# Kernel tuning notes

Measured on AMD Instinct MI355X. Metric: run time of the kernel, lower is better.

The kernel has to match this reference:

```python
import jax, jax.numpy as jnp
import numpy as np
from jax import lax

L = 2048        # leaves per tree
VOCAB = 50000
IN_DIM = 300
MEM = 150
HID = 50
NCLS = 5


def _balanced_tree(n_leaf):
    # children-before-parent topological order; node ids: [0, n_leaf) leaves,
    # [n_leaf, 2*n_leaf-1) internal, last id is the root's single child (ROOT is passthrough).
    level = list(range(n_leaf)); nid = n_leaf; lefts = []; rights = []
    while len(level) > 1:
        nxt = []
        for j in range(0, len(level) - 1, 2):
            lefts.append(level[j]); rights.append(level[j + 1]); nxt.append(nid); nid += 1
        if len(level) % 2:
            nxt.append(level[-1])
        level = nxt
    return np.asarray(lefts, np.int32), np.asarray(rights, np.int32)


def setup_inputs() -> dict:
    key = jax.random.key(0)
    ks = jax.random.split(key, 12)
    left, right = _balanced_tree(L)
    s = 0.05
    return {
        "l_tokens": jax.random.randint(ks[0], (L,), 0, VOCAB, dtype=jnp.int32),
        "r_tokens": jax.random.randint(ks[1], (L,), 0, VOCAB, dtype=jnp.int32),
        "left_idx": jnp.asarray(left),
        "right_idx": jnp.asarray(right),
        "emb": jax.random.normal(ks[2], (VOCAB, IN_DIM), jnp.float32) * s,
        "W_ioux": jax.random.normal(ks[3], (IN_DIM, 3 * MEM), jnp.float32) * s,
        "b_ioux": jnp.zeros((3 * MEM,), jnp.float32),
        "W_iouh": jax.random.normal(ks[4], (MEM, 3 * MEM), jnp.float32) * s,
        "b_iouh": jnp.zeros((3 * MEM,), jnp.float32),
        "W_fx": jax.random.normal(ks[5], (IN_DIM, MEM), jnp.float32) * s,
        "b_fx": jnp.zeros((MEM,), jnp.float32),
        "W_fh": jax.random.normal(ks[6], (MEM, MEM), jnp.float32) * s,
        "b_fh": jnp.zeros((MEM,), jnp.float32),
        "W_attn": jax.random.normal(ks[7], (2 * MEM, MEM), jnp.float32) * s,
        "b_attn": jnp.zeros((MEM,), jnp.float32),
        "W_wh": jax.random.normal(ks[8], (2 * MEM, HID), jnp.float32) * s,
        "b_wh": jnp.zeros((HID,), jnp.float32),
        "W_wp": jax.random.normal(ks[9], (HID, NCLS), jnp.float32) * s,
        "b_wp": jnp.zeros((NCLS,), jnp.float32),
    }


def _gates(iou):
    i, o, u = jnp.split(iou, 3, axis=-1)
    return jax.nn.sigmoid(i), jax.nn.sigmoid(o), jnp.tanh(u)


def _tree_lstm(tokens, left, right, emb, W_ioux, b_ioux, W_iouh, b_iouh, W_fh, b_fh):
    # Leaves (child_c = child_h = 0): iou = ioux(x) + iouh(0); fc term vanishes.
    x = emb[tokens]                                   # [L, in_dim]
    i, o, u = _gates(x @ W_ioux + b_ioux + b_iouh)
    c_leaf = i * u
    h_leaf = o * jnp.tanh(c_leaf)
    n_leaf = tokens.shape[0]
    N = 2 * n_leaf - 1
    C = jnp.zeros((N, MEM), x.dtype).at[:n_leaf].set(c_leaf)
    H = jnp.zeros((N, MEM), x.dtype).at[:n_leaf].set(h_leaf)

    # Internal nodes (inputs=None branch): iou = iouh(sum h_child); f_k = sigmoid(fh(h_k)).
    def step(carry, inp):
        C, H = carry
        k, li, ri = inp
        hl, hr = H[li], H[ri]
        i, o, u = _gates((hl + hr) @ W_iouh + b_iouh)
        fl = jax.nn.sigmoid(hl @ W_fh + b_fh)
        fr = jax.nn.sigmoid(hr @ W_fh + b_fh)
        c = i * u + fl * C[li] + fr * C[ri]
        h = o * jnp.tanh(c)
        return (C.at[k].set(c), H.at[k].set(h)), None

    ids = jnp.arange(n_leaf, N, dtype=jnp.int32)
    (C, H), _ = lax.scan(step, (C, H), (ids, left, right))
    return H  # [N, MEM]; H[-1] is the root hidden state (ROOT is passthrough)


def reference(l_tokens, r_tokens, left_idx, right_idx, emb, W_ioux, b_ioux, W_iouh, b_iouh, W_fx, b_fx, W_fh, b_fh, W_attn, b_attn, W_wh, b_wh, W_wp, b_wp):
    Hl = _tree_lstm(l_tokens, left_idx, right_idx, emb, W_ioux, b_ioux, W_iouh, b_iouh, W_fh, b_fh)
    Hr = _tree_lstm(r_tokens, left_idx, right_idx, emb, W_ioux, b_ioux, W_iouh, b_iouh, W_fh, b_fh)
    # Soft cross-attention over all node hidden states (torch code builds [Nr,Nl,m] beta;
    # here expressed as matmuls -- identical math).
    scores = Hl @ Hr.T                               # [Nl, Nr]
    beta_sum = jax.nn.softmax(scores, axis=1) @ Hr    # [Nl, MEM]
    alpha_sum = jax.nn.softmax(scores.T, axis=1) @ Hl  # [Nr, MEM]
    v_l = jnp.concatenate([Hl, beta_sum], axis=1) @ W_attn + b_attn
    v_r = jnp.concatenate([Hr, alpha_sum], axis=1) @ W_attn + b_attn
    lh = v_l[-1:]  # root hidden (root_idx is the root's matched row)
    rh = v_r[-1:]
    feats = jnp.concatenate([lh * rh, jnp.abs(lh - rh)], axis=1)
    hid = jax.nn.sigmoid(feats @ W_wh + b_wh)
    return jax.nn.log_softmax(hid @ W_wp + b_wp, axis=-1)  # [1, NCLS]
```

## Files before the change

kernel.cpp:

```cpp
#include <hip/hip_runtime.h>
#include <math.h>

#define LEAVES 2048
#define NN     4095
#define MEMD   150
#define IOUD   450
#define IND    300
#define STR    152
#define CT     4096


__device__ __forceinline__ float sigf(float x) { return 1.f / (1.f + expf(-x)); }

__global__ __launch_bounds__(256) void k_pack(
    const float* __restrict__ Wh, const float* __restrict__ Wf,
    float4* __restrict__ PWhf)
{
    int i = blockIdx.x * 256 + threadIdx.x;
    if (i < 22500) {
        int k = i / 150, d = i - k * 150;
        float4 v;
        v.x = Wh[k * IOUD + d];
        v.y = Wh[k * IOUD + 150 + d];
        v.z = Wh[k * IOUD + 300 + d];
        v.w = Wf[k * MEMD + d];
        PWhf[i] = v;
    }
}

__global__ __launch_bounds__(320) void k_leaf(
    const int* __restrict__ ltok, const int* __restrict__ rtok,
    const float* __restrict__ emb, const float* __restrict__ Wx,
    const float* __restrict__ bx, const float* __restrict__ bh,
    float* __restrict__ C, float* __restrict__ H)
{
    __shared__ __align__(16) float xs[IND][4];
    __shared__ int tok[4];
    const int tree = blockIdx.y, t = threadIdx.x;
    const int leaf0 = blockIdx.x << 2;
    const int* toks = tree ? rtok : ltok;

    if (t < 4) tok[t] = toks[leaf0 + t];
    __syncthreads();
    if (t < 300) {
        int q = t >> 2, m = t & 3;
        float4 v = *(const float4*)(emb + (size_t)tok[m] * IND + 4 * q);
        xs[4*q+0][m] = v.x; xs[4*q+1][m] = v.y;
        xs[4*q+2][m] = v.z; xs[4*q+3][m] = v.w;
    }
    __syncthreads();

    const int lane = t & 63, w = t >> 6;
    const int kh = lane >> 5;
    const int d  = w * 32 + (lane & 31);
    const bool act = (d < 150);

    float ai[4] = {0.f,0.f,0.f,0.f};
    float ao[4] = {0.f,0.f,0.f,0.f};
    float au[4] = {0.f,0.f,0.f,0.f};

    const float* wp = Wx + (act ? d : 0);
    const int kb = kh * 150;
    #pragma unroll 5
    for (int kk = 0; kk < 150; ++kk) {
        const int k = kb + kk;
        float wi = wp[k * IOUD];
        float wo = wp[k * IOUD + 150];
        float wu = wp[k * IOUD + 300];
        float4 x4 = *(const float4*)(&xs[k][0]);
        float xv[4] = {x4.x, x4.y, x4.z, x4.w};
        #pragma unroll
        for (int m = 0; m < 4; ++m) {
            ai[m] = fmaf(xv[m], wi, ai[m]);
            ao[m] = fmaf(xv[m], wo, ao[m]);
            au[m] = fmaf(xv[m], wu, au[m]);
        }
    }

    #pragma unroll
    for (int m = 0; m < 4; ++m) {
        ai[m] += __shfl_xor(ai[m], 32);
        ao[m] += __shfl_xor(ao[m], 32);
        au[m] += __shfl_xor(au[m], 32);
    }

    if (act && kh == 0) {
        const float bi = bx[d]       + bh[d];
        const float bo = bx[d + 150] + bh[d + 150];
        const float bu = bx[d + 300] + bh[d + 300];
        float* Ct = C + ((size_t)tree * CT + leaf0) * STR;
        float* Ht = H + ((size_t)tree * CT + leaf0) * STR;
        #pragma unroll
        for (int m = 0; m < 4; ++m) {
            float c = sigf(ai[m] + bi) * tanhf(au[m] + bu);
            float h = sigf(ao[m] + bo) * tanhf(c);
            Ct[(size_t)m * STR + d] = c;
            Ht[(size_t)m * STR + d] = h;
        }
    }
}

__global__ __launch_bounds__(640) void k_lvl(
    const float4* __restrict__ PWhf, const float* __restrict__ bh,
    const float* __restrict__ bf,
    float* __restrict__ C, float* __restrict__ H, int PB, int CB)
{
    __shared__ float buf[MEMD][8];
    __shared__ float pb[300][11];
    const int tree = blockIdx.y, t = threadIdx.x;
    const int p0 = blockIdx.x * 4;
    float* Ct = C + (size_t)tree * CT * STR;
    float* Ht = H + (size_t)tree * CT * STR;

    if (t < 600) {
        int m = t / 150, d2 = t - m * 150;
        int cc = CB + 2 * (p0 + m);
        float a = Ht[(size_t)cc * STR + d2];
        float b = Ht[(size_t)(cc + 1) * STR + d2];
        buf[d2][2*m + 0] = a + b;
        buf[d2][2*m + 1] = a;
    }
    __syncthreads();

    const int kh = (t >= 320) ? 1 : 0;
    const int tt = t - 320 * kh;
    const bool act = (tt < 300);
    const int hf = (tt >= 150) ? 1 : 0;
    const int d  = tt - 150 * hf;
    const int m0 = hf * 2;

    float ai[2], ao[2], au[2], afs[2], afl[2], cl[2], cr[2];
    if (act) {
        if (kh == 0) {
            const float bi = bh[d], bo = bh[d + 150], bu = bh[d + 300], bfv = bf[d];
            #pragma unroll
            for (int m = 0; m < 2; ++m) {
                ai[m] = bi; ao[m] = bo; au[m] = bu;
                afs[m] = 2.f * bfv; afl[m] = bfv;
                int cc = CB + 2 * (p0 + m0 + m);
                cl[m] = Ct[(size_t)cc * STR + d];
                cr[m] = Ct[(size_t)(cc + 1) * STR + d];
            }
        } else {
            #pragma unroll
            for (int m = 0; m < 2; ++m) {
                ai[m] = 0.f; ao[m] = 0.f; au[m] = 0.f; afs[m] = 0.f; afl[m] = 0.f;
            }
        }
        const float4* wp = PWhf + d;
        const int kb = kh * 75;
        #pragma unroll 5
        for (int kk = 0; kk < 75; ++kk) {
            const int k = kb + kk;
            float4 w = wp[(size_t)k * 150];
            float4 p4 = *(const float4*)(&buf[k][2 * m0]);
            float hs0 = p4.x, hl0 = p4.y, hs1 = p4.z, hl1 = p4.w;
            ai[0]  = fmaf(hs0, w.x, ai[0]);   ai[1]  = fmaf(hs1, w.x, ai[1]);
            ao[0]  = fmaf(hs0, w.y, ao[0]);   ao[1]  = fmaf(hs1, w.y, ao[1]);
            au[0]  = fmaf(hs0, w.z, au[0]);   au[1]  = fmaf(hs1, w.z, au[1]);
            afs[0] = fmaf(hs0, w.w, afs[0]);  afs[1] = fmaf(hs1, w.w, afs[1]);
            afl[0] = fmaf(hl0, w.w, afl[0]);  afl[1] = fmaf(hl1, w.w, afl[1]);
        }
    }
    if (kh == 1 && act) {
        #pragma unroll
        for (int m = 0; m < 2; ++m) {
            pb[tt][5*m + 0] = ai[m];
            pb[tt][5*m + 1] = ao[m];
            pb[tt][5*m + 2] = au[m];
            pb[tt][5*m + 3] = afs[m];
            pb[tt][5*m + 4] = afl[m];
        }
    }
    __syncthreads();
    if (kh == 0 && act) {
        #pragma unroll
        for (int m = 0; m < 2; ++m) {
            float aiv  = ai[m]  + pb[tt][5*m + 0];
            float aov  = ao[m]  + pb[tt][5*m + 1];
            float auv  = au[m]  + pb[tt][5*m + 2];
            float afsv = afs[m] + pb[tt][5*m + 3];
            float aflv = afl[m] + pb[tt][5*m + 4];
            float frv = afsv - aflv;
            float c = sigf(aiv) * tanhf(auv) + sigf(aflv) * cl[m] + sigf(frv) * cr[m];
            float h = sigf(aov) * tanhf(c);
            size_t rw = (size_t)(PB + p0 + m0 + m) * STR + d;
            Ct[rw] = c;
            Ht[rw] = h;
        }
    }
}

__global__ __launch_bounds__(640) void k_node(
    const float4* __restrict__ PWhf, const float* __restrict__ bh,
    const float* __restrict__ bf,
    float* __restrict__ C, float* __restrict__ H, int PB, int CB)
{
    __shared__ float hsv[MEMD], hlv[MEMD];
    __shared__ float part[4][5][152];
    const int tree = blockIdx.y, node = blockIdx.x, t = threadIdx.x;
    float* Ct = C + (size_t)tree * CT * STR;
    float* Ht = H + (size_t)tree * CT * STR;
    const int c0 = CB + 2 * node;

    if (t < MEMD) {
        float a = Ht[(size_t)c0 * STR + t];
        float b = Ht[(size_t)(c0 + 1) * STR + t];
        hsv[t] = a + b;
        hlv[t] = a;
    }
    __syncthreads();

    const int grp = t / 160, d = t - grp * 160;
    if (d < MEMD) {
        const int k0 = (grp * MEMD) >> 2;
        const int k1 = ((grp + 1) * MEMD) >> 2;
        float ai = 0.f, ao = 0.f, au = 0.f, afs = 0.f, afl = 0.f;
        const float4* wp = PWhf + d;
        #pragma unroll 4
        for (int k = k0; k < k1; ++k) {
            float4 w = wp[(size_t)k * 150];
            float hs = hsv[k], hl = hlv[k];
            ai  = fmaf(hs, w.x, ai);
            ao  = fmaf(hs, w.y, ao);
            au  = fmaf(hs, w.z, au);
            afs = fmaf(hs, w.w, afs);
            afl = fmaf(hl, w.w, afl);
        }
        part[grp][0][d] = ai;  part[grp][1][d] = ao;  part[grp][2][d] = au;
        part[grp][3][d] = afs; part[grp][4][d] = afl;
    }
    __syncthreads();

    if (t < MEMD) {
        const int d2 = t;
        float ai = bh[d2], ao = bh[d2 + 150], au = bh[d2 + 300];
        float bfv = bf[d2];
        float afs = 2.f * bfv, afl = bfv;
        #pragma unroll
        for (int g = 0; g < 4; ++g) {
            ai  += part[g][0][d2]; ao  += part[g][1][d2]; au += part[g][2][d2];
            afs += part[g][3][d2]; afl += part[g][4][d2];
        }
        float cl = Ct[(size_t)c0 * STR + d2];
        float cr = Ct[(size_t)(c0 + 1) * STR + d2];
        float frv = afs - afl;
        float c = sigf(ai) * tanhf(au) + sigf(afl) * cl + sigf(frv) * cr;
        float h = sigf(ao) * tanhf(c);
        size_t rw = (size_t)(PB + node) * STR + d2;
        Ct[rw] = c;
        Ht[rw] = h;
    }
}

__global__ __launch_bounds__(256) void k_attn(
    const float* __restrict__ H, float* __restrict__ cstat, float* __restrict__ part)
{
    __shared__ float lv[MEMD];
    __shared__ float sc[64];
    __shared__ float pv[64];
    const int bid = blockIdx.x, t = threadIdx.x;
    const int side = bid >> 6, chunk = bid & 63;
    const int j0 = chunk << 6;
    const int jn = min(64, NN - j0);
    const float* lastrow = H + ((size_t)side * CT + (NN - 1)) * STR;
    if (t < MEMD) lv[t] = lastrow[t];
    __syncthreads();

    const float* src = H + (size_t)(side ^ 1) * CT * STR + (size_t)j0 * STR;
    const int wave = t >> 6, lane = t & 63;
    for (int r = wave; r < jn; r += 4) {
        const float* row = src + (size_t)r * STR;
        float a = lv[lane] * row[lane] + lv[lane + 64] * row[lane + 64];
        if (lane < 22) a += lv[lane + 128] * row[lane + 128];
        #pragma unroll
        for (int off = 32; off; off >>= 1) a += __shfl_xor(a, off);
        if (lane == 0) sc[r] = a;
    }
    __syncthreads();
    if (wave == 0) {
        float v = (lane < jn) ? sc[lane] : -3.4e38f;
        float m = v;
        #pragma unroll
        for (int off = 32; off; off >>= 1) m = fmaxf(m, __shfl_xor(m, off));
        float e = (lane < jn) ? expf(v - m) : 0.f;
        pv[lane] = e;
        float s = e;
        #pragma unroll
        for (int off = 32; off; off >>= 1) s += __shfl_xor(s, off);
        if (lane == 0) {
            cstat[(side * 64 + chunk) * 2 + 0] = m;
            cstat[(side * 64 + chunk) * 2 + 1] = s;
        }
    }
    __syncthreads();
    if (t < MEMD) {
        float a = 0.f;
        for (int j = 0; j < jn; ++j) a += pv[j] * src[(size_t)j * STR + t];
        part[(size_t)(side * 64 + chunk) * STR + t] = a;
    }
}

__global__ __launch_bounds__(512) void k_final(
    const float* __restrict__ H, const float* __restrict__ cstat,
    const float* __restrict__ part,
    const float* __restrict__ Wattn, const float* __restrict__ battn,
    const float* __restrict__ Wwh, const float* __restrict__ bwh,
    const float* __restrict__ Wwp, const float* __restrict__ bwp,
    float* __restrict__ outp)
{
    __shared__ float scl[2][64];
    __shared__ float gseS[2];
    __shared__ float ba[300], catl[300], catr[300], vl[150], vr[150];
    __shared__ float feats[300], hid[50], logits[5];
    const int t = threadIdx.x, wave = t >> 6, lane = t & 63;

    if (wave < 2) {
        float lm = cstat[(wave * 64 + lane) * 2 + 0];
        float ls = cstat[(wave * 64 + lane) * 2 + 1];
        float m = lm;
        #pragma unroll
        for (int off = 32; off; off >>= 1) m = fmaxf(m, __shfl_xor(m, off));
        float s = expf(lm - m);
        scl[wave][lane] = s;
        float se = ls * s;
        #pragma unroll
        for (int off = 32; off; off >>= 1) se += __shfl_xor(se, off);
        if (lane == 0) gseS[wave] = se;
    }
    __syncthreads();
    if (t < 300) {
        int side = t / MEMD, d = t - side * MEMD;
        float a = 0.f;
        for (int c = 0; c < 64; ++c)
            a += part[(size_t)(side * 64 + c) * STR + d] * scl[side][c];
        ba[t] = a / gseS[side];
    }
    __syncthreads();
    const float* Hl_last = H + (size_t)(0 * CT + NN - 1) * STR;
    const float* Hr_last = H + (size_t)(1 * CT + NN - 1) * STR;
    if (t < MEMD) {
        catl[t] = Hl_last[t]; catl[150 + t] = ba[t];
        catr[t] = Hr_last[t]; catr[150 + t] = ba[150 + t];
    }
    __syncthreads();
    if (t < 300) {
        int d = (t < 150) ? t : t - 150;
        const float* cat = (t < 150) ? catl : catr;
        float a = battn[d];
        for (int k = 0; k < 300; ++k) a = fmaf(cat[k], Wattn[k * 150 + d], a);
        if (t < 150) vl[d] = a; else vr[d] = a;
    }
    __syncthreads();
    if (t < MEMD) {
        feats[t] = vl[t] * vr[t];
        feats[150 + t] = fabsf(vl[t] - vr[t]);
    }
    __syncthreads();
    if (t < 50) {
        float a = bwh[t];
        for (int k = 0; k < 300; ++k) a = fmaf(feats[k], Wwh[k * 50 + t], a);
        hid[t] = sigf(a);
    }
    __syncthreads();
    if (t < 5) {
        float a = bwp[t];
        for (int g = 0; g < 50; ++g) a = fmaf(hid[g], Wwp[g * 5 + t], a);
        logits[t] = a;
    }
    __syncthreads();
    if (t == 0) {
        float m = logits[0];
        for (int c = 1; c < 5; ++c) m = fmaxf(m, logits[c]);
        float s = 0.f;
        for (int c = 0; c < 5; ++c) s += expf(logits[c] - m);
        float lse = m + logf(s);
        for (int c = 0; c < 5; ++c) outp[c] = logits[c] - lse;
    }
}

extern "C" void kernel_launch(void* const* d_in, const int* in_sizes, int n_in,
                              void* d_out, int out_size, void* d_ws, size_t ws_size,
                              hipStream_t stream)
{
    const int*   ltok  = (const int*)d_in[0];
    const int*   rtok  = (const int*)d_in[1];
    const float* emb   = (const float*)d_in[4];
    const float* Wx    = (const float*)d_in[5];
    const float* bx    = (const float*)d_in[6];
    const float* Wh    = (const float*)d_in[7];
    const float* bh    = (const float*)d_in[8];
    const float* Wf    = (const float*)d_in[11];
    const float* bf    = (const float*)d_in[12];
    const float* Wattn = (const float*)d_in[13];
    const float* battn = (const float*)d_in[14];
    const float* Wwh   = (const float*)d_in[15];
    const float* bwh   = (const float*)d_in[16];
    const float* Wwp   = (const float*)d_in[17];
    const float* bwp   = (const float*)d_in[18];
    float* out = (float*)d_out;

    float* ws    = (float*)d_ws;
    float*  C    = ws;
    float*  H    = C + (size_t)2 * CT * STR;
    float*  cs   = H + (size_t)2 * CT * STR;
    float*  part = cs + 256;
    float4* PWhf = (float4*)(part + (size_t)128 * STR);

    k_pack<<<dim3(88), dim3(256), 0, stream>>>(Wh, Wf, PWhf);

    k_leaf<<<dim3(512, 2), dim3(320), 0, stream>>>(ltok, rtok, emb, Wx, bx, bh, C, H);

    k_lvl<<<dim3(256, 2), dim3(640), 0, stream>>>(PWhf, bh, bf, C, H, 2048, 0);
    k_lvl<<<dim3(128, 2), dim3(640), 0, stream>>>(PWhf, bh, bf, C, H, 3072, 2048);
    k_lvl<<<dim3(64,  2), dim3(640), 0, stream>>>(PWhf, bh, bf, C, H, 3584, 3072);

    k_node<<<dim3(128, 2), dim3(640), 0, stream>>>(PWhf, bh, bf, C, H, 3840, 3584);
    k_node<<<dim3(64,  2), dim3(640), 0, stream>>>(PWhf, bh, bf, C, H, 3968, 3840);
    k_node<<<dim3(32,  2), dim3(640), 0, stream>>>(PWhf, bh, bf, C, H, 4032, 3968);
    k_node<<<dim3(16,  2), dim3(640), 0, stream>>>(PWhf, bh, bf, C, H, 4064, 4032);
    k_node<<<dim3(8,   2), dim3(640), 0, stream>>>(PWhf, bh, bf, C, H, 4080, 4064);
    k_node<<<dim3(4,   2), dim3(640), 0, stream>>>(PWhf, bh, bf, C, H, 4088, 4080);
    k_node<<<dim3(2,   2), dim3(640), 0, stream>>>(PWhf, bh, bf, C, H, 4092, 4088);
    k_node<<<dim3(1,   2), dim3(640), 0, stream>>>(PWhf, bh, bf, C, H, 4094, 4092);

    k_attn<<<dim3(128), dim3(256), 0, stream>>>(H, cs, part);
    k_final<<<dim3(1), dim3(512), 0, stream>>>(H, cs, part, Wattn, battn,
                                               Wwh, bwh, Wwp, bwp, out);
}
```

Measured before the change: 155.3 us.

## Compute leaf input projection as bf16 MFMA GEMM with separate activation pass

Replaces the fused fp32 leaf kernel with a pipeline: pack Wx into bf16 MFMA B-fragment layout, gather and convert token embeddings to bf16, run a 16x16x32 bf16 MFMA GEMM into an fp32 IOU buffer, then apply the gate activations in a separate kernel. The aim is to move the 4096x300x450 leaf projection from scalar FMAs onto the matrix cores. In exchange it adds two extra launches and an intermediate IOU round trip through global memory, and lowers input precision to bf16, which may affect accuracy.

```diff
diff --git a/kernel.cpp b/kernel.cpp
--- a/kernel.cpp
+++ b/kernel.cpp
@@ -8,13 +8,25 @@
 #define IND    300
 #define STR    152
 #define CT     4096
-
+#define NT     29
+#define KT     10
+#define IOUSTR 464
 
 __device__ __forceinline__ float sigf(float x) { return 1.f / (1.f + expf(-x)); }
 
-__global__ __launch_bounds__(256) void k_pack(
+__device__ __forceinline__ unsigned short f2bf(float v) {
+    union { float f; unsigned u; } x; x.f = v;
+    unsigned r = x.u + 0x7fffu + ((x.u >> 16) & 1u);
+    return (unsigned short)(r >> 16);
+}
+
+typedef short bf16x8 __attribute__((ext_vector_type(8)));
+typedef float f32x4  __attribute__((ext_vector_type(4)));
+
+__global__ __launch_bounds__(256) void k_pack2(
     const float* __restrict__ Wh, const float* __restrict__ Wf,
-    float4* __restrict__ PWhf)
+    const float* __restrict__ Wx,
+    float4* __restrict__ PWhf, unsigned short* __restrict__ PB)
 {
     int i = blockIdx.x * 256 + threadIdx.x;
     if (i < 22500) {
@@ -25,85 +37,94 @@
         v.z = Wh[k * IOUD + 300 + d];
         v.w = Wf[k * MEMD + d];
         PWhf[i] = v;
-    }
-}
-
-__global__ __launch_bounds__(320) void k_leaf(
+    } else if (i < 22500 + NT * KT * 64) {
+        int j2 = i - 22500;
+        int nt = j2 / (KT * 64);
+        int rem = j2 - nt * (KT * 64);
+        int kt = rem >> 6, l = rem & 63;
+        int jc = nt * 16 + (l & 15);
+        int kb = kt * 32 + ((l >> 4) << 3);
+        unsigned short o[8];
+        #pragma unroll
+        for (int e = 0; e < 8; ++e) {
+            int k = kb + e;
+            float v = (k < IND && jc < IOUD) ? Wx[k * IOUD + jc] : 0.f;
+            o[e] = f2bf(v);
+        }
+        *(ushort4*)(PB + (size_t)j2 * 8)     = make_ushort4(o[0], o[1], o[2], o[3]);
+        *(ushort4*)(PB + (size_t)j2 * 8 + 4) = make_ushort4(o[4], o[5], o[6], o[7]);
+    }
+}
+
+__global__ __launch_bounds__(256) void k_prepx(
     const int* __restrict__ ltok, const int* __restrict__ rtok,
-    const float* __restrict__ emb, const float* __restrict__ Wx,
+    const float* __restrict__ emb, unsigned short* __restrict__ Xb)
+{
+    int idx = blockIdx.x * 256 + threadIdx.x;
+    if (idx >= 4096 * 80) return;
+    int row = idx / 80, q = idx - row * 80;
+    int kb = q * 4;
+    int leaf = row & 2047, tree = row >> 11;
+    int tk = (tree ? rtok : ltok)[leaf];
+    unsigned short o[4];
+    #pragma unroll
+    for (int e = 0; e < 4; ++e) {
+        int k = kb + e;
+        float v = (k < IND) ? emb[(size_t)tk * IND + k] : 0.f;
+        o[e] = f2bf(v);
+    }
+    *(ushort4*)(Xb + (size_t)row * 320 + kb) = make_ushort4(o[0], o[1], o[2], o[3]);
+}
+
+__global__ __launch_bounds__(256) void k_gemm(
+    const unsigned short* __restrict__ Xb, const unsigned short* __restrict__ PB,
+    float* __restrict__ IOU)
+{
+    const int wave = threadIdx.x >> 6, l = threadIdx.x & 63;
+    const int tid = blockIdx.x * 4 + wave;
+    const int mt = tid / NT, nt = tid - mt * NT;
+
+    const short* Ap = (const short*)Xb + (size_t)(mt * 16 + (l & 15)) * 320 + ((l >> 4) << 3);
+    const short* Bp = (const short*)PB + (size_t)nt * (KT * 512) + l * 8;
+
+    f32x4 acc = {0.f, 0.f, 0.f, 0.f};
+    #pragma unroll
+    for (int kt = 0; kt < KT; ++kt) {
+        bf16x8 a = *(const bf16x8*)(Ap + kt * 32);
+        bf16x8 b = *(const bf16x8*)(Bp + kt * 512);
+        acc = __builtin_amdgcn_mfma_f32_16x16x32_bf16(a, b, acc, 0, 0, 0);
+    }
+
+    const int col = nt * 16 + (l & 15);
+    const int rb  = mt * 16 + ((l >> 4) << 2);
+    #pragma unroll
+    for (int r = 0; r < 4; ++r)
+        IOU[(size_t)(rb + r) * IOUSTR + col] = acc[r];
+}
+
+__global__ __launch_bounds__(256) void k_act(
+    const float* __restrict__ IOU,
     const float* __restrict__ bx, const float* __restrict__ bh,
     float* __restrict__ C, float* __restrict__ H)
 {
-    __shared__ __align__(16) float xs[IND][4];
-    __shared__ int tok[4];
-    const int tree = blockIdx.y, t = threadIdx.x;
-    const int leaf0 = blockIdx.x << 2;
-    const int* toks = tree ? rtok : ltok;
-
-    if (t < 4) tok[t] = toks[leaf0 + t];
-    __syncthreads();
-    if (t < 300) {
-        int q = t >> 2, m = t & 3;
-        float4 v = *(const float4*)(emb + (size_t)tok[m] * IND + 4 * q);
-        xs[4*q+0][m] = v.x; xs[4*q+1][m] = v.y;
-        xs[4*q+2][m] = v.z; xs[4*q+3][m] = v.w;
-    }
-    __syncthreads();
-
-    const int lane = t & 63, w = t >> 6;
-    const int kh = lane >> 5;
-    const int d  = w * 32 + (lane & 31);
-    const bool act = (d < 150);
-
-    float ai[4] = {0.f,0.f,0.f,0.f};
-    float ao[4] = {0.f,0.f,0.f,0.f};
-    float au[4] = {0.f,0.f,0.f,0.f};
-
-    const float* wp = Wx + (act ? d : 0);
-    const int kb = kh * 150;
-    #pragma unroll 5
-    for (int kk = 0; kk < 150; ++kk) {
-        const int k = kb + kk;
-        float wi = wp[k * IOUD];
-        float wo = wp[k * IOUD + 150];
-        float wu = wp[k * IOUD + 300];
-        float4 x4 = *(const float4*)(&xs[k][0]);
-        float xv[4] = {x4.x, x4.y, x4.z, x4.w};
-        #pragma unroll
-        for (int m = 0; m < 4; ++m) {
-            ai[m] = fmaf(xv[m], wi, ai[m]);
-            ao[m] = fmaf(xv[m], wo, ao[m]);
-            au[m] = fmaf(xv[m], wu, au[m]);
-        }
-    }
-
-    #pragma unroll
-    for (int m = 0; m < 4; ++m) {
-        ai[m] += __shfl_xor(ai[m], 32);
-        ao[m] += __shfl_xor(ao[m], 32);
-        au[m] += __shfl_xor(au[m], 32);
-    }
-
-    if (act && kh == 0) {
-        const float bi = bx[d]       + bh[d];
-        const float bo = bx[d + 150] + bh[d + 150];
-        const float bu = bx[d + 300] + bh[d + 300];
-        float* Ct = C + ((size_t)tree * CT + leaf0) * STR;
-        float* Ht = H + ((size_t)tree * CT + leaf0) * STR;
-        #pragma unroll
-        for (int m = 0; m < 4; ++m) {
-            float c = sigf(ai[m] + bi) * tanhf(au[m] + bu);
-            float h = sigf(ao[m] + bo) * tanhf(c);
-            Ct[(size_t)m * STR + d] = c;
-            Ht[(size_t)m * STR + d] = h;
-        }
-    }
+    int idx = blockIdx.x * 256 + threadIdx.x;
+    if (idx >= 4096 * 150) return;
+    int m = idx / 150, d = idx - m * 150;
+    const float* r = IOU + (size_t)m * IOUSTR;
+    float iv = r[d]       + bx[d]       + bh[d];
+    float ov = r[d + 150] + bx[d + 150] + bh[d + 150];
+    float uv = r[d + 300] + bx[d + 300] + bh[d + 300];
+    float c = sigf(iv) * tanhf(uv);
+    float h = sigf(ov) * tanhf(c);
+    int tree = m >> 11, leaf = m & 2047;
+    C[((size_t)tree * CT + leaf) * STR + d] = c;
+    H[((size_t)tree * CT + leaf) * STR + d] = h;
 }
 
 __global__ __launch_bounds__(640) void k_lvl(
     const float4* __restrict__ PWhf, const float* __restrict__ bh,
     const float* __restrict__ bf,
-    float* __restrict__ C, float* __restrict__ H, int PB, int CB)
+    float* __restrict__ C, float* __restrict__ H, int PB_, int CB)
 {
     __shared__ float buf[MEMD][8];
     __shared__ float pb[300][11];
@@ -184,7 +205,7 @@
             float frv = afsv - aflv;
             float c = sigf(aiv) * tanhf(auv) + sigf(aflv) * cl[m] + sigf(frv) * cr[m];
             float h = sigf(aov) * tanhf(c);
-            size_t rw = (size_t)(PB + p0 + m0 + m) * STR + d;
+            size_t rw = (size_t)(PB_ + p0 + m0 + m) * STR + d;
             Ct[rw] = c;
             Ht[rw] = h;
         }
@@ -194,7 +215,7 @@
 __global__ __launch_bounds__(640) void k_node(
     const float4* __restrict__ PWhf, const float* __restrict__ bh,
     const float* __restrict__ bf,
-    float* __restrict__ C, float* __restrict__ H, int PB, int CB)
+    float* __restrict__ C, float* __restrict__ H, int PB_, int CB)
 {
     __shared__ float hsv[MEMD], hlv[MEMD];
     __shared__ float part[4][5][152];
@@ -247,7 +268,7 @@
         float frv = afs - afl;
         float c = sigf(ai) * tanhf(au) + sigf(afl) * cl + sigf(frv) * cr;
         float h = sigf(ao) * tanhf(c);
-        size_t rw = (size_t)(PB + node) * STR + d2;
+        size_t rw = (size_t)(PB_ + node) * STR + d2;
         Ct[rw] = c;
         Ht[rw] = h;
     }
@@ -406,10 +427,14 @@
     float*  cs   = H + (size_t)2 * CT * STR;
     float*  part = cs + 256;
     float4* PWhf = (float4*)(part + (size_t)128 * STR);
-
-    k_pack<<<dim3(88), dim3(256), 0, stream>>>(Wh, Wf, PWhf);
-
-    k_leaf<<<dim3(512, 2), dim3(320), 0, stream>>>(ltok, rtok, emb, Wx, bx, bh, C, H);
+    float*  IOU  = (float*)(PWhf + 22500);
+    unsigned short* Xb = (unsigned short*)(IOU + (size_t)4096 * IOUSTR);
+    unsigned short* PBb = Xb + (size_t)4096 * 320;
+
+    k_pack2<<<dim3(161), dim3(256), 0, stream>>>(Wh, Wf, Wx, PWhf, PBb);
+    k_prepx<<<dim3(1280), dim3(256), 0, stream>>>(ltok, rtok, emb, Xb);
+    k_gemm<<<dim3(256 * NT / 4), dim3(256), 0, stream>>>(Xb, PBb, IOU);
+    k_act<<<dim3(2400), dim3(256), 0, stream>>>(IOU, bx, bh, C, H);
 
     k_lvl<<<dim3(256, 2), dim3(640), 0, stream>>>(PWhf, bh, bf, C, H, 2048, 0);
     k_lvl<<<dim3(128, 2), dim3(640), 0, stream>>>(PWhf, bh, bf, C, H, 3072, 2048);
```

Result: faster. 143.8 us (-7.4%).
